# Performance work log

Measured on AMD Instinct MI355X. Metric: run time of the kernel, lower is better.

The kernel has to match this reference:

```python
import jax, jax.numpy as jnp
import numpy as np

N = 100000   # nodes
E = 1600000  # edges (before self-loops)
F_IN = 128
H = 64
G = 512      # graphs in batch


def _add_self_loops(edge_index, n):
    loop = jnp.arange(n, dtype=edge_index.dtype)
    src = jnp.concatenate([edge_index[0], loop])
    dst = jnp.concatenate([edge_index[1], loop])
    return src, dst


def _gcn_norm(src, dst, n):
    # PyG GCNConv: deg over targets with self-loops, norm = d^-1/2[src]*d^-1/2[dst]
    deg = jax.ops.segment_sum(jnp.ones_like(dst, dtype=jnp.float32), dst, num_segments=n)
    dinv = jnp.where(deg > 0, jax.lax.rsqrt(deg), 0.0)
    return dinv[src] * dinv[dst]


def _gcn_conv(x, src, dst, norm, W, b):
    xw = x @ W                                # [N, H]
    msg = xw[src] * norm[:, None]             # [E+N, H] gather + scale
    out = jax.ops.segment_sum(msg, dst, num_segments=x.shape[0])
    return out + b


def setup_inputs() -> dict:
    key = jax.random.key(0)
    ks = jax.random.split(key, 9)
    x = jax.random.normal(ks[0], (N, F_IN), dtype=jnp.float32)
    edge_index = jax.random.randint(ks[1], (2, E), 0, N, dtype=jnp.int32)
    batch = jnp.sort(jax.random.randint(ks[2], (N,), 0, G, dtype=jnp.int32))
    s1 = 1.0 / np.sqrt(F_IN)
    s2 = 1.0 / np.sqrt(H)
    W1 = jax.random.uniform(ks[3], (F_IN, H), jnp.float32, -s1, s1)
    b1 = jnp.zeros((H,), jnp.float32)
    W2 = jax.random.uniform(ks[4], (H, H), jnp.float32, -s2, s2)
    b2 = jnp.zeros((H,), jnp.float32)
    Wl = jax.random.uniform(ks[5], (H, 1), jnp.float32, -s2, s2)
    bl = jnp.zeros((1,), jnp.float32)
    return {"x": x, "edge_index": edge_index, "batch": batch,
            "W1": W1, "b1": b1, "W2": W2, "b2": b2, "Wl": Wl, "bl": bl}


def reference(x, edge_index, batch, W1, b1, W2, b2, Wl, bl):
    n = x.shape[0]
    src, dst = _add_self_loops(edge_index, n)
    norm = _gcn_norm(src, dst, n)
    h = jax.nn.relu(_gcn_conv(x, src, dst, norm, W1, b1))
    h = jax.nn.relu(_gcn_conv(h, src, dst, norm, W2, b2))
    # global mean pool over graphs
    sums = jax.ops.segment_sum(h, batch, num_segments=G)          # [G, H]
    cnt = jax.ops.segment_sum(jnp.ones((n,), jnp.float32), batch, num_segments=G)
    pooled = sums / jnp.maximum(cnt, 1.0)[:, None]
    return jax.nn.sigmoid(pooled @ Wl + bl)                        # [G, 1]
```

## Files before the change

### kernel.cpp

```cpp
#include <hip/hip_runtime.h>
#include <hip/hip_bf16.h>
#include <cmath>

#define F_IN 128
#define HDIM 64
#define NPB 256
#define NB1 512
#define CAP 4800
#define CHMAX 3136

typedef __attribute__((ext_vector_type(8))) short bf16x8;
typedef __attribute__((ext_vector_type(4))) float f32x4;
typedef __attribute__((ext_vector_type(2))) float f32x2;

__device__ __forceinline__ float bf2f(unsigned short u) {
    union { unsigned int i; float f; } v; v.i = ((unsigned int)u) << 16; return v.f;
}
__device__ __forceinline__ unsigned short f2bf(float f) {
    __hip_bfloat16 h = __float2bfloat16(f);
    union { __hip_bfloat16 h; unsigned short u; } c; c.h = h; return c.u;
}
__device__ __forceinline__ unsigned char f2fp8(float f) {
    int p = __builtin_amdgcn_cvt_pk_fp8_f32(f, f, 0, false);
    return (unsigned char)(p & 0xff);
}
__device__ __forceinline__ void fp8x8_acc(uint2 v, float* a) {
    f32x2 f;
    f = __builtin_amdgcn_cvt_pk_f32_fp8(v.x, false); a[0] += f.x; a[1] += f.y;
    f = __builtin_amdgcn_cvt_pk_f32_fp8(v.x, true);  a[2] += f.x; a[3] += f.y;
    f = __builtin_amdgcn_cvt_pk_f32_fp8(v.y, false); a[4] += f.x; a[5] += f.y;
    f = __builtin_amdgcn_cvt_pk_f32_fp8(v.y, true);  a[6] += f.x; a[7] += f.y;
}
__device__ __forceinline__ void fp8x8_acc_m(uint2 v, float m, float* a) {
    f32x2 f;
    f = __builtin_amdgcn_cvt_pk_f32_fp8(v.x, false); a[0] = fmaf(f.x, m, a[0]); a[1] = fmaf(f.y, m, a[1]);
    f = __builtin_amdgcn_cvt_pk_f32_fp8(v.x, true);  a[2] = fmaf(f.x, m, a[2]); a[3] = fmaf(f.y, m, a[3]);
    f = __builtin_amdgcn_cvt_pk_f32_fp8(v.y, false); a[4] = fmaf(f.x, m, a[4]); a[5] = fmaf(f.y, m, a[5]);
    f = __builtin_amdgcn_cvt_pk_f32_fp8(v.y, true);  a[6] = fmaf(f.x, m, a[6]); a[7] = fmaf(f.y, m, a[7]);
}

__device__ __forceinline__ void gather_rows(const int* __restrict__ col,
                                            const uint2* __restrict__ xws,
                                            int L, int s, int end, float* a) {
    int e = s;
    for (; e + 8 <= end; e += 8) {
        uint2 v0 = xws[(size_t)col[e + 0] * 8 + L];
        uint2 v1 = xws[(size_t)col[e + 1] * 8 + L];
        uint2 v2 = xws[(size_t)col[e + 2] * 8 + L];
        uint2 v3 = xws[(size_t)col[e + 3] * 8 + L];
        uint2 v4 = xws[(size_t)col[e + 4] * 8 + L];
        uint2 v5 = xws[(size_t)col[e + 5] * 8 + L];
        uint2 v6 = xws[(size_t)col[e + 6] * 8 + L];
        uint2 v7 = xws[(size_t)col[e + 7] * 8 + L];
        fp8x8_acc(v0, a); fp8x8_acc(v1, a); fp8x8_acc(v2, a); fp8x8_acc(v3, a);
        fp8x8_acc(v4, a); fp8x8_acc(v5, a); fp8x8_acc(v6, a); fp8x8_acc(v7, a);
    }
    if (e < end) {
        int last = end - 1;
        uint2 v0 = xws[(size_t)col[e]               * 8 + L];
        uint2 v1 = xws[(size_t)col[min(e + 1, last)] * 8 + L];
        uint2 v2 = xws[(size_t)col[min(e + 2, last)] * 8 + L];
        uint2 v3 = xws[(size_t)col[min(e + 3, last)] * 8 + L];
        uint2 v4 = xws[(size_t)col[min(e + 4, last)] * 8 + L];
        uint2 v5 = xws[(size_t)col[min(e + 5, last)] * 8 + L];
        uint2 v6 = xws[(size_t)col[min(e + 6, last)] * 8 + L];
        uint2 v7 = xws[(size_t)col[min(e + 7, last)] * 8 + L];
        fp8x8_acc(v0, a);
        fp8x8_acc_m(v1, (e + 1 < end) ? 1.0f : 0.0f, a);
        fp8x8_acc_m(v2, (e + 2 < end) ? 1.0f : 0.0f, a);
        fp8x8_acc_m(v3, (e + 3 < end) ? 1.0f : 0.0f, a);
        fp8x8_acc_m(v4, (e + 4 < end) ? 1.0f : 0.0f, a);
        fp8x8_acc_m(v5, (e + 5 < end) ? 1.0f : 0.0f, a);
        fp8x8_acc_m(v6, (e + 6 < end) ? 1.0f : 0.0f, a);
        fp8x8_acc_m(v7, (e + 7 < end) ? 1.0f : 0.0f, a);
    }
}


__launch_bounds__(256)
__global__ void k_init(const float* __restrict__ W1, const float* __restrict__ W2,
                       unsigned short* __restrict__ w1t, unsigned short* __restrict__ w2t,
                       const int* __restrict__ batch, int* __restrict__ gstart,
                       int n, int G, int* __restrict__ gcnt) {
    int t = blockIdx.x * 256 + threadIdx.x;
    if (t < F_IN * 64) {
        int c = t & 63, k = t >> 6;
        w1t[c * F_IN + k] = f2bf(W1[t]);
        return;
    }
    t -= F_IN * 64;
    if (t < HDIM * 64) {
        int c = t & 63, k = t >> 6;
        w2t[c * HDIM + k] = f2bf(W2[t]);
        return;
    }
    t -= HDIM * 64;
    if (t <= G) {
        int g = t;
        int lo = 0, hi = n;
        while (lo < hi) {
            int mid = (lo + hi) >> 1;
            if (batch[mid] < g) lo = mid + 1; else hi = mid;
        }
        gstart[g] = lo;
        return;
    }
    t -= G + 1;
    if (t < 512) gcnt[t] = 0;
}


__launch_bounds__(512)
__global__ void p_place(const int* __restrict__ src, const int* __restrict__ dst,
                        int* __restrict__ gcnt, int* __restrict__ pairs,
                        int E, int nbuk, int chunk) {
    __shared__ int hist[512];
    __shared__ int cur[512];
    __shared__ int dch[CHMAX];
    int tid = threadIdx.x;
    for (int i = tid; i < nbuk; i += 512) hist[i] = 0;
    __syncthreads();
    int lo = blockIdx.x * chunk, hi = min(E, lo + chunk), m = hi - lo;
    for (int i = tid; i < m; i += 512) {
        int d = dst[lo + i];
        dch[i] = d;
        atomicAdd(&hist[d >> 8], 1);
    }
    __syncthreads();
    for (int i = tid; i < nbuk; i += 512) {
        int c = hist[i];
        cur[i] = i * CAP + (c ? atomicAdd(&gcnt[i], c) : 0);
    }
    __syncthreads();
    for (int i = tid; i < m; i += 512) {
        int d = dch[i];
        int pos = atomicAdd(&cur[d >> 8], 1);
        pairs[pos] = (src[lo + i] << 8) | (d & 255);
    }
}


__launch_bounds__(256)
__global__ void p2_csr(const int* __restrict__ pairs, const int* __restrict__ bucket_cnt,
                       float* __restrict__ dinv, int* __restrict__ col,
                       int4* __restrict__ slot_hdr, int n) {
    __shared__ int plds[CAP];
    __shared__ int dl[256];
    __shared__ int sc[256];
    __shared__ int cur[256];
    __shared__ int h64[64];
    __shared__ int s64[64];
    int b = blockIdx.x, tid = threadIdx.x;
    int nlo = b << 8;
    int eb = b * CAP;
    int cnt = bucket_cnt[b];
    dl[tid] = 0;
    if (tid < 64) h64[tid] = 0;
    __syncthreads();
    for (int i = tid; i < cnt; i += 256) {
        int v = pairs[eb + i];
        plds[i] = v;
        atomicAdd(&dl[v & 255], 1);
    }
    __syncthreads();
    int d0 = dl[tid];
    sc[tid] = d0;
    __syncthreads();
    for (int off = 1; off < 256; off <<= 1) {
        int a = (tid >= off) ? sc[tid - off] : 0;
        __syncthreads();
        sc[tid] += a;
        __syncthreads();
    }
    int excl = sc[tid] - d0;
    int node = nlo + tid;
    float dv = rsqrtf((float)(d0 + 1));
    if (node < n) dinv[node] = dv;
    cur[tid] = eb + excl;
    atomicAdd(&h64[min(d0, 63)], 1);
    __syncthreads();
    if (tid == 0) { int run = 0; for (int i = 0; i < 64; ++i) { s64[i] = run; run += h64[i]; } }
    __syncthreads();
    if (tid < 64) h64[tid] = 0;
    __syncthreads();
    {
        int bin = min(d0, 63);
        int pos = s64[bin] + atomicAdd(&h64[bin], 1);
        int4 hdr;
        hdr.x = (node < n) ? node : 0x7fffffff;
        hdr.y = eb + excl;
        hdr.z = d0;
        hdr.w = __float_as_int(dv);
        slot_hdr[nlo + pos] = hdr;
    }
    __syncthreads();
    for (int i = tid; i < cnt; i += 256) {
        unsigned int v = (unsigned int)plds[i];
        int pos = atomicAdd(&cur[v & 255], 1);
        col[pos] = (int)(v >> 8);
    }
}


template <int K>
__launch_bounds__(256)
__global__ void matmul_mfma(const float* __restrict__ X, const unsigned short* __restrict__ Wt,
                            const float* __restrict__ dinv, unsigned char* __restrict__ out,
                            int n) {
    constexpr int KS  = K / 32;
    constexpr int LDX = K + 8;
    __shared__ unsigned short Xs[64 * LDX];
    __shared__ unsigned short Ws[64 * LDX];
    int tid = threadIdx.x;
    int rowbase = blockIdx.x * 64;
    for (int i = tid; i < 64 * (K / 8); i += 256) {
        int r = i / (K / 8), ch = i % (K / 8);
        *(bf16x8*)(Ws + r * LDX + ch * 8) = ((const bf16x8*)Wt)[i];
    }
    {
        const float4* X4 = (const float4*)X;
        for (int i = tid; i < 64 * (K / 4); i += 256) {
            int r = i / (K / 4), k4 = i % (K / 4);
            ushort4 u = { 0, 0, 0, 0 };
            int gr = rowbase + r;
            if (gr < n) {
                float4 v = X4[(size_t)gr * (K / 4) + k4];
                u.x = f2bf(v.x); u.y = f2bf(v.y); u.z = f2bf(v.z); u.w = f2bf(v.w);
            }
            *(ushort4*)(Xs + r * LDX + k4 * 4) = u;
        }
    }
    __syncthreads();
    int wave = tid >> 6, lane = tid & 63;
    int q = lane >> 4, nn = lane & 15;
    f32x4 acc[4] = {{0,0,0,0},{0,0,0,0},{0,0,0,0},{0,0,0,0}};
    int mrow = wave * 16 + nn;
#pragma unroll
    for (int s = 0; s < KS; ++s) {
        bf16x8 af = *(const bf16x8*)(Xs + mrow * LDX + s * 32 + q * 8);
#pragma unroll
        for (int c = 0; c < 4; ++c) {
            bf16x8 bf = *(const bf16x8*)(Ws + (c * 16 + nn) * LDX + s * 32 + q * 8);
            acc[c] = __builtin_amdgcn_mfma_f32_16x16x32_bf16(af, bf, acc[c], 0, 0, 0);
        }
    }
#pragma unroll
    for (int r = 0; r < 4; ++r) {
        int row = rowbase + wave * 16 + q * 4 + r;
        if (row >= n) continue;
        float dv = dinv[row];
#pragma unroll
        for (int c = 0; c < 4; ++c)
            out[(size_t)row * HDIM + c * 16 + nn] = f2fp8(acc[c][r] * dv);
    }
}


__launch_bounds__(256)
__global__ void gather1_mm2(const int4* __restrict__ slot_hdr, const int* __restrict__ col,
                            const uint2* __restrict__ xws, const float* __restrict__ bias,
                            const unsigned short* __restrict__ w2t,
                            unsigned char* __restrict__ out8, int nslots, int n) {
    __shared__ unsigned short Hs[32 * 72];
    __shared__ unsigned short Ws[64 * 72];
    __shared__ int   snode[32];
    __shared__ float sdinv[32];

    int tid = threadIdx.x;
    int ls = tid >> 3;
    int L  = tid & 7;
    int slot = blockIdx.x * 32 + ls;

    for (int i = tid; i < 64 * 8; i += 256) {
        int r = i >> 3, ch = i & 7;
        *(bf16x8*)(Ws + r * 72 + ch * 8) = ((const bf16x8*)w2t)[i];
    }

    int node = 0x7fffffff;
    float dv = 0.0f;
    float a[8] = {0, 0, 0, 0, 0, 0, 0, 0};
    if (slot < nslots) {
        int4 hdr = slot_hdr[slot];
        node = hdr.x;
        if (node < n) {
            dv = __int_as_float(hdr.w);
            fp8x8_acc(xws[(size_t)node * 8 + L], a);
            gather_rows(col, xws, L, hdr.y, hdr.y + hdr.z, a);
        }
    }
    if (L == 0) { snode[ls] = node; sdinv[ls] = dv; }
    {
        int f0 = L * 8;
        bf16x8 o;
        if (node < n) {
#pragma unroll
            for (int j = 0; j < 8; ++j)
                o[j] = (short)f2bf(fmaxf(fmaf(a[j], dv, bias[f0 + j]), 0.0f));
        } else {
            short z[8] = {0,0,0,0,0,0,0,0};
            o = *(bf16x8*)z;
        }
        *(bf16x8*)(Hs + ls * 72 + L * 8) = o;
    }
    __syncthreads();

    int wave = tid >> 6, lane = tid & 63;
    int q = lane >> 4, nn = lane & 15;
    int mt  = wave & 1;
    int nt0 = (wave >> 1) * 2;
    f32x4 acc[2] = {{0,0,0,0},{0,0,0,0}};
#pragma unroll
    for (int s = 0; s < 2; ++s) {
        bf16x8 af = *(const bf16x8*)(Hs + (mt * 16 + nn) * 72 + s * 32 + q * 8);
#pragma unroll
        for (int t = 0; t < 2; ++t) {
            bf16x8 bf = *(const bf16x8*)(Ws + ((nt0 + t) * 16 + nn) * 72 + s * 32 + q * 8);
            acc[t] = __builtin_amdgcn_mfma_f32_16x16x32_bf16(af, bf, acc[t], 0, 0, 0);
        }
    }
#pragma unroll
    for (int r = 0; r < 4; ++r) {
        int lslot = mt * 16 + q * 4 + r;
        int nd = snode[lslot];
        if (nd >= n) continue;
        float dvr = sdinv[lslot];
#pragma unroll
        for (int t = 0; t < 2; ++t)
            out8[(size_t)nd * HDIM + (nt0 + t) * 16 + nn] = f2fp8(acc[t][r] * dvr);
    }
}


__launch_bounds__(256)
__global__ void csr_gather8_fp8(const int4* __restrict__ slot_hdr, const int* __restrict__ col,
                                const uint2* __restrict__ xws, const float* __restrict__ bias,
                                bf16x8* __restrict__ outb, int nslots, int n) {
    int t = blockIdx.x * 256 + threadIdx.x;
    int slot = t >> 3;
    if (slot >= nslots) return;
    int L = t & 7;
    int4 hdr = slot_hdr[slot];
    int node = hdr.x;
    if (node >= n) return;
    float dv = __int_as_float(hdr.w);

    float a[8] = {0, 0, 0, 0, 0, 0, 0, 0};
    fp8x8_acc(xws[(size_t)node * 8 + L], a);
    gather_rows(col, xws, L, hdr.y, hdr.y + hdr.z, a);

    int f0 = L * 8;
    bf16x8 o;
#pragma unroll
    for (int j = 0; j < 8; ++j)
        o[j] = (short)f2bf(fmaxf(fmaf(a[j], dv, bias[f0 + j]), 0.0f));
    outb[(size_t)node * 8 + L] = o;
}


__launch_bounds__(256)
__global__ void pool_head(const unsigned short* __restrict__ h, const int* __restrict__ gstart,
                          const float* __restrict__ Wl, const float* __restrict__ bl,
                          float* __restrict__ out, int G) {
    int g = blockIdx.x;
    int s = gstart[g], e = gstart[g + 1];
    int f  = threadIdx.x & 63;
    int rg = threadIdx.x >> 6;
    float acc = 0.0f;
    for (int i = s + rg; i < e; i += 4)
        acc += bf2f(h[(size_t)i * HDIM + f]);
    __shared__ float red[4][HDIM];
    red[rg][f] = acc;
    __syncthreads();
    if (rg == 0) {
        float v = (red[0][f] + red[1][f]) + (red[2][f] + red[3][f]);
        float c = fmaxf((float)(e - s), 1.0f);
        v = v * Wl[f] * (1.0f / c);
#pragma unroll
        for (int off = 32; off; off >>= 1) v += __shfl_down(v, off, 64);
        if (f == 0) out[g] = 1.0f / (1.0f + expf(-(v + bl[0])));
    }
}


extern "C" void kernel_launch(void* const* d_in, const int* in_sizes, int n_in,
                              void* d_out, int out_size, void* d_ws, size_t ws_size,
                              hipStream_t stream) {
    const float* x   = (const float*)d_in[0];
    const int* ei    = (const int*)d_in[1];
    const int* batch = (const int*)d_in[2];
    const float* W1  = (const float*)d_in[3];
    const float* b1  = (const float*)d_in[4];
    const float* W2  = (const float*)d_in[5];
    const float* b2  = (const float*)d_in[6];
    const float* Wl  = (const float*)d_in[7];
    const float* bl  = (const float*)d_in[8];
    float* out = (float*)d_out;

    const int n = in_sizes[0] / F_IN;
    const int E = in_sizes[1] / 2;
    const int G = out_size;

    const int* srcp = ei;
    const int* dstp = ei + E;

    int nbuk = (n + NPB - 1) / NPB;
    int nslots = nbuk * NPB;

    char* wsb = (char*)d_ws;
    auto alloc = [&](size_t bytes) { char* p = wsb; wsb += (bytes + 255) & ~(size_t)255; return p; };
    float* dinv       = (float*)alloc((size_t)n * 4);
    int4*  slot_hdr   = (int4*)alloc((size_t)nslots * 16);
    int*   gcnt       = (int*)alloc(512 * 4);
    int*   pairs      = (int*)alloc((size_t)nbuk * CAP * 4);
    int*   colx       = (int*)alloc((size_t)nbuk * CAP * 4);
    unsigned short* w1t  = (unsigned short*)alloc((size_t)F_IN * HDIM * 2);
    unsigned short* w2t  = (unsigned short*)alloc((size_t)HDIM * HDIM * 2);
    unsigned char*  xws8 = (unsigned char*)alloc((size_t)n * HDIM);
    unsigned char*  xws8b= (unsigned char*)alloc((size_t)n * HDIM);
    unsigned short* xh2  = (unsigned short*)alloc((size_t)n * HDIM * 2);
    int*   gstart     = (int*)alloc(((size_t)G + 1) * 4);

    const int TB = 256;
    int gMM  = (n + 63) / 64;
    int chunk = (E + NB1 - 1) / NB1;
    int gG8  = (nslots * 8 + TB - 1) / TB;
    int gS   = (nslots + 31) / 32;
    int initWork = F_IN * 64 + HDIM * 64 + (G + 1) + 512;
    int gInit = (initWork + TB - 1) / TB;

    k_init<<<gInit, TB, 0, stream>>>(W1, W2, w1t, w2t, batch, gstart, n, G, gcnt);
    p_place<<<NB1, 512, 0, stream>>>(srcp, dstp, gcnt, pairs, E, nbuk, chunk);
    p2_csr<<<nbuk, TB, 0, stream>>>(pairs, gcnt, dinv, colx, slot_hdr, n);
    matmul_mfma<F_IN><<<gMM, TB, 0, stream>>>(x, w1t, dinv, xws8, n);
    gather1_mm2<<<gS, TB, 0, stream>>>(slot_hdr, colx, (const uint2*)xws8,
                                       b1, w2t, xws8b, nslots, n);
    csr_gather8_fp8<<<gG8, TB, 0, stream>>>(slot_hdr, colx, (const uint2*)xws8b,
                                            b2, (bf16x8*)xh2, nslots, n);
    pool_head<<<G, TB, 0, stream>>>(xh2, gstart, Wl, bl, out, G);
}
```

Measured before the change: 230.9 us.

## Fuse all GCN stages into one persistent cooperative kernel with grid syncs

Replaces seven separate kernel launches with a single cooperative persistent kernel that runs each stage (init, bucket placement, CSR build, layer-1 matmul, gather+matmul2, gather2, pooling) in grid-stride loops separated by grid.sync(). The goal is to remove per-launch overhead and inter-kernel gaps. As part of the fusion, the first matmul reads X directly from global memory into registers instead of staging it in LDS, and the placement pass now uses 1024 chunks with 256 threads. The trade-offs are a shared LDS union that may limit occupancy, a grid size capped by co-residency, and grid-wide barrier costs between stages.

```diff
diff --git a/kernel.cpp b/kernel.cpp
--- a/kernel.cpp
+++ b/kernel.cpp
@@ -1,13 +1,16 @@
 #include <hip/hip_runtime.h>
+#include <hip/hip_cooperative_groups.h>
 #include <hip/hip_bf16.h>
 #include <cmath>
+
+namespace cg = cooperative_groups;
 
 #define F_IN 128
 #define HDIM 64
 #define NPB 256
-#define NB1 512
+#define NCH 1024
 #define CAP 4800
-#define CHMAX 3136
+#define CHMAX 1600
 
 typedef __attribute__((ext_vector_type(8))) short bf16x8;
 typedef __attribute__((ext_vector_type(4))) float f32x4;
@@ -57,7 +60,7 @@
     }
     if (e < end) {
         int last = end - 1;
-        uint2 v0 = xws[(size_t)col[e]               * 8 + L];
+        uint2 v0 = xws[(size_t)col[e]                * 8 + L];
         uint2 v1 = xws[(size_t)col[min(e + 1, last)] * 8 + L];
         uint2 v2 = xws[(size_t)col[min(e + 2, last)] * 8 + L];
         uint2 v3 = xws[(size_t)col[min(e + 3, last)] * 8 + L];
@@ -76,308 +79,282 @@
     }
 }
 
-
-__launch_bounds__(256)
-__global__ void k_init(const float* __restrict__ W1, const float* __restrict__ W2,
-                       unsigned short* __restrict__ w1t, unsigned short* __restrict__ w2t,
-                       const int* __restrict__ batch, int* __restrict__ gstart,
-                       int n, int G, int* __restrict__ gcnt) {
-    int t = blockIdx.x * 256 + threadIdx.x;
-    if (t < F_IN * 64) {
-        int c = t & 63, k = t >> 6;
-        w1t[c * F_IN + k] = f2bf(W1[t]);
-        return;
-    }
-    t -= F_IN * 64;
-    if (t < HDIM * 64) {
-        int c = t & 63, k = t >> 6;
-        w2t[c * HDIM + k] = f2bf(W2[t]);
-        return;
-    }
-    t -= HDIM * 64;
-    if (t <= G) {
-        int g = t;
-        int lo = 0, hi = n;
-        while (lo < hi) {
-            int mid = (lo + hi) >> 1;
-            if (batch[mid] < g) lo = mid + 1; else hi = mid;
-        }
-        gstart[g] = lo;
-        return;
-    }
-    t -= G + 1;
-    if (t < 512) gcnt[t] = 0;
-}
-
-
-__launch_bounds__(512)
-__global__ void p_place(const int* __restrict__ src, const int* __restrict__ dst,
-                        int* __restrict__ gcnt, int* __restrict__ pairs,
-                        int E, int nbuk, int chunk) {
-    __shared__ int hist[512];
-    __shared__ int cur[512];
-    __shared__ int dch[CHMAX];
-    int tid = threadIdx.x;
-    for (int i = tid; i < nbuk; i += 512) hist[i] = 0;
-    __syncthreads();
-    int lo = blockIdx.x * chunk, hi = min(E, lo + chunk), m = hi - lo;
-    for (int i = tid; i < m; i += 512) {
-        int d = dst[lo + i];
-        dch[i] = d;
-        atomicAdd(&hist[d >> 8], 1);
-    }
-    __syncthreads();
-    for (int i = tid; i < nbuk; i += 512) {
-        int c = hist[i];
-        cur[i] = i * CAP + (c ? atomicAdd(&gcnt[i], c) : 0);
-    }
-    __syncthreads();
-    for (int i = tid; i < m; i += 512) {
-        int d = dch[i];
-        int pos = atomicAdd(&cur[d >> 8], 1);
-        pairs[pos] = (src[lo + i] << 8) | (d & 255);
-    }
-}
-
-
-__launch_bounds__(256)
-__global__ void p2_csr(const int* __restrict__ pairs, const int* __restrict__ bucket_cnt,
-                       float* __restrict__ dinv, int* __restrict__ col,
-                       int4* __restrict__ slot_hdr, int n) {
-    __shared__ int plds[CAP];
-    __shared__ int dl[256];
-    __shared__ int sc[256];
-    __shared__ int cur[256];
-    __shared__ int h64[64];
-    __shared__ int s64[64];
-    int b = blockIdx.x, tid = threadIdx.x;
-    int nlo = b << 8;
-    int eb = b * CAP;
-    int cnt = bucket_cnt[b];
-    dl[tid] = 0;
-    if (tid < 64) h64[tid] = 0;
-    __syncthreads();
-    for (int i = tid; i < cnt; i += 256) {
-        int v = pairs[eb + i];
-        plds[i] = v;
-        atomicAdd(&dl[v & 255], 1);
-    }
-    __syncthreads();
-    int d0 = dl[tid];
-    sc[tid] = d0;
-    __syncthreads();
-    for (int off = 1; off < 256; off <<= 1) {
-        int a = (tid >= off) ? sc[tid - off] : 0;
-        __syncthreads();
-        sc[tid] += a;
-        __syncthreads();
-    }
-    int excl = sc[tid] - d0;
-    int node = nlo + tid;
-    float dv = rsqrtf((float)(d0 + 1));
-    if (node < n) dinv[node] = dv;
-    cur[tid] = eb + excl;
-    atomicAdd(&h64[min(d0, 63)], 1);
-    __syncthreads();
-    if (tid == 0) { int run = 0; for (int i = 0; i < 64; ++i) { s64[i] = run; run += h64[i]; } }
-    __syncthreads();
-    if (tid < 64) h64[tid] = 0;
-    __syncthreads();
+struct GcnP {
+    const float* x; const int* src; const int* dst; const int* batch;
+    const float* W1; const float* b1; const float* W2; const float* b2;
+    const float* Wl; const float* bl; float* out;
+    float* dinv; int4* slot_hdr; int* gcnt; int* pairs; int* col;
+    unsigned short* w1t; unsigned short* w2t;
+    unsigned char* xws8; unsigned char* xws8b; unsigned short* xh2;
+    int* gstart;
+    int n, E, G, nbuk, nslots, chunk;
+};
+
+union SU {
+    struct { int hist[512], cur[512], dch[CHMAX]; } p1;
+    struct { int plds[CAP], dl[256], sc[256], cur[256], h64[64], s64[64]; } p2;
+    struct { unsigned short Ws[64 * 136]; } p3;
+    struct { unsigned short Ws[64 * 72], Hs[32 * 72]; int snode[32]; float sdinv[32]; } p4;
+    struct { float red[4][HDIM]; } p6;
+};
+
+__launch_bounds__(256, 4)
+__global__ void gcn_fused(GcnP p) {
+    cg::grid_group grid = cg::this_grid();
+    __shared__ SU su;
+    const int tid = threadIdx.x;
+    const int nbuk = p.nbuk;
+
     {
-        int bin = min(d0, 63);
-        int pos = s64[bin] + atomicAdd(&h64[bin], 1);
-        int4 hdr;
-        hdr.x = (node < n) ? node : 0x7fffffff;
-        hdr.y = eb + excl;
-        hdr.z = d0;
-        hdr.w = __float_as_int(dv);
-        slot_hdr[nlo + pos] = hdr;
-    }
-    __syncthreads();
-    for (int i = tid; i < cnt; i += 256) {
-        unsigned int v = (unsigned int)plds[i];
-        int pos = atomicAdd(&cur[v & 255], 1);
-        col[pos] = (int)(v >> 8);
-    }
-}
-
-
-template <int K>
-__launch_bounds__(256)
-__global__ void matmul_mfma(const float* __restrict__ X, const unsigned short* __restrict__ Wt,
-                            const float* __restrict__ dinv, unsigned char* __restrict__ out,
-                            int n) {
-    constexpr int KS  = K / 32;
-    constexpr int LDX = K + 8;
-    __shared__ unsigned short Xs[64 * LDX];
-    __shared__ unsigned short Ws[64 * LDX];
-    int tid = threadIdx.x;
-    int rowbase = blockIdx.x * 64;
-    for (int i = tid; i < 64 * (K / 8); i += 256) {
-        int r = i / (K / 8), ch = i % (K / 8);
-        *(bf16x8*)(Ws + r * LDX + ch * 8) = ((const bf16x8*)Wt)[i];
-    }
+        int total = F_IN * 64 + HDIM * 64 + (p.G + 1) + 512;
+        for (int t = blockIdx.x * 256 + tid; t < total; t += gridDim.x * 256) {
+            int u = t;
+            if (u < F_IN * 64) { int c = u & 63, k = u >> 6; p.w1t[c * F_IN + k] = f2bf(p.W1[u]); continue; }
+            u -= F_IN * 64;
+            if (u < HDIM * 64) { int c = u & 63, k = u >> 6; p.w2t[c * HDIM + k] = f2bf(p.W2[u]); continue; }
+            u -= HDIM * 64;
+            if (u <= p.G) {
+                int g = u, lo = 0, hi = p.n;
+                while (lo < hi) { int mid = (lo + hi) >> 1; if (p.batch[mid] < g) lo = mid + 1; else hi = mid; }
+                p.gstart[g] = lo;
+                continue;
+            }
+            u -= p.G + 1;
+            if (u < 512) p.gcnt[u] = 0;
+        }
+    }
+    grid.sync();
+
+    for (int c = blockIdx.x; c < NCH; c += gridDim.x) {
+        for (int i = tid; i < nbuk; i += 256) su.p1.hist[i] = 0;
+        __syncthreads();
+        int lo = c * p.chunk, hi = min(p.E, lo + p.chunk), m = hi - lo;
+        for (int i = tid; i < m; i += 256) {
+            int d = p.dst[lo + i];
+            su.p1.dch[i] = d;
+            atomicAdd(&su.p1.hist[d >> 8], 1);
+        }
+        __syncthreads();
+        for (int i = tid; i < nbuk; i += 256) {
+            int cc = su.p1.hist[i];
+            su.p1.cur[i] = i * CAP + (cc ? atomicAdd(&p.gcnt[i], cc) : 0);
+        }
+        __syncthreads();
+        for (int i = tid; i < m; i += 256) {
+            int d = su.p1.dch[i];
+            int pos = atomicAdd(&su.p1.cur[d >> 8], 1);
+            p.pairs[pos] = (p.src[lo + i] << 8) | (d & 255);
+        }
+        __syncthreads();
+    }
+    grid.sync();
+
+    for (int b = blockIdx.x; b < nbuk; b += gridDim.x) {
+        int nlo = b << 8;
+        int eb = b * CAP;
+        int cnt = p.gcnt[b];
+        su.p2.dl[tid] = 0;
+        if (tid < 64) su.p2.h64[tid] = 0;
+        __syncthreads();
+        for (int i = tid; i < cnt; i += 256) {
+            int v = p.pairs[eb + i];
+            su.p2.plds[i] = v;
+            atomicAdd(&su.p2.dl[v & 255], 1);
+        }
+        __syncthreads();
+        int d0 = su.p2.dl[tid];
+        su.p2.sc[tid] = d0;
+        __syncthreads();
+        for (int off = 1; off < 256; off <<= 1) {
+            int a = (tid >= off) ? su.p2.sc[tid - off] : 0;
+            __syncthreads();
+            su.p2.sc[tid] += a;
+            __syncthreads();
+        }
+        int excl = su.p2.sc[tid] - d0;
+        int node = nlo + tid;
+        float dv = rsqrtf((float)(d0 + 1));
+        if (node < p.n) p.dinv[node] = dv;
+        su.p2.cur[tid] = eb + excl;
+        atomicAdd(&su.p2.h64[min(d0, 63)], 1);
+        __syncthreads();
+        if (tid == 0) { int run = 0; for (int i = 0; i < 64; ++i) { su.p2.s64[i] = run; run += su.p2.h64[i]; } }
+        __syncthreads();
+        if (tid < 64) su.p2.h64[tid] = 0;
+        __syncthreads();
+        {
+            int bin = min(d0, 63);
+            int pos = su.p2.s64[bin] + atomicAdd(&su.p2.h64[bin], 1);
+            int4 hdr;
+            hdr.x = (node < p.n) ? node : 0x7fffffff;
+            hdr.y = eb + excl;
+            hdr.z = d0;
+            hdr.w = __float_as_int(dv);
+            p.slot_hdr[nlo + pos] = hdr;
+        }
+        __syncthreads();
+        for (int i = tid; i < cnt; i += 256) {
+            unsigned int v = (unsigned int)su.p2.plds[i];
+            int pos = atomicAdd(&su.p2.cur[v & 255], 1);
+            p.col[pos] = (int)(v >> 8);
+        }
+        __syncthreads();
+    }
+    grid.sync();
+
     {
-        const float4* X4 = (const float4*)X;
-        for (int i = tid; i < 64 * (K / 4); i += 256) {
-            int r = i / (K / 4), k4 = i % (K / 4);
-            ushort4 u = { 0, 0, 0, 0 };
-            int gr = rowbase + r;
-            if (gr < n) {
-                float4 v = X4[(size_t)gr * (K / 4) + k4];
-                u.x = f2bf(v.x); u.y = f2bf(v.y); u.z = f2bf(v.z); u.w = f2bf(v.w);
-            }
-            *(ushort4*)(Xs + r * LDX + k4 * 4) = u;
-        }
-    }
-    __syncthreads();
-    int wave = tid >> 6, lane = tid & 63;
-    int q = lane >> 4, nn = lane & 15;
-    f32x4 acc[4] = {{0,0,0,0},{0,0,0,0},{0,0,0,0},{0,0,0,0}};
-    int mrow = wave * 16 + nn;
-#pragma unroll
-    for (int s = 0; s < KS; ++s) {
-        bf16x8 af = *(const bf16x8*)(Xs + mrow * LDX + s * 32 + q * 8);
-#pragma unroll
-        for (int c = 0; c < 4; ++c) {
-            bf16x8 bf = *(const bf16x8*)(Ws + (c * 16 + nn) * LDX + s * 32 + q * 8);
-            acc[c] = __builtin_amdgcn_mfma_f32_16x16x32_bf16(af, bf, acc[c], 0, 0, 0);
-        }
-    }
-#pragma unroll
-    for (int r = 0; r < 4; ++r) {
-        int row = rowbase + wave * 16 + q * 4 + r;
-        if (row >= n) continue;
-        float dv = dinv[row];
-#pragma unroll
-        for (int c = 0; c < 4; ++c)
-            out[(size_t)row * HDIM + c * 16 + nn] = f2fp8(acc[c][r] * dv);
-    }
-}
-
-
-__launch_bounds__(256)
-__global__ void gather1_mm2(const int4* __restrict__ slot_hdr, const int* __restrict__ col,
-                            const uint2* __restrict__ xws, const float* __restrict__ bias,
-                            const unsigned short* __restrict__ w2t,
-                            unsigned char* __restrict__ out8, int nslots, int n) {
-    __shared__ unsigned short Hs[32 * 72];
-    __shared__ unsigned short Ws[64 * 72];
-    __shared__ int   snode[32];
-    __shared__ float sdinv[32];
-
-    int tid = threadIdx.x;
-    int ls = tid >> 3;
-    int L  = tid & 7;
-    int slot = blockIdx.x * 32 + ls;
-
-    for (int i = tid; i < 64 * 8; i += 256) {
-        int r = i >> 3, ch = i & 7;
-        *(bf16x8*)(Ws + r * 72 + ch * 8) = ((const bf16x8*)w2t)[i];
-    }
-
-    int node = 0x7fffffff;
-    float dv = 0.0f;
-    float a[8] = {0, 0, 0, 0, 0, 0, 0, 0};
-    if (slot < nslots) {
-        int4 hdr = slot_hdr[slot];
-        node = hdr.x;
-        if (node < n) {
-            dv = __int_as_float(hdr.w);
-            fp8x8_acc(xws[(size_t)node * 8 + L], a);
-            gather_rows(col, xws, L, hdr.y, hdr.y + hdr.z, a);
-        }
-    }
-    if (L == 0) { snode[ls] = node; sdinv[ls] = dv; }
+        int gMM = (p.n + 63) >> 6;
+        int wave = tid >> 6, lane = tid & 63, q = lane >> 4, nn = lane & 15;
+        for (int tile = blockIdx.x; tile < gMM; tile += gridDim.x) {
+            for (int i = tid; i < 64 * 16; i += 256) {
+                int r = i >> 4, ch = i & 15;
+                *(bf16x8*)(su.p3.Ws + r * 136 + ch * 8) = ((const bf16x8*)p.w1t)[i];
+            }
+            __syncthreads();
+            int rowbase = tile << 6;
+            int arow = rowbase + wave * 16 + nn;
+            bool rok = arow < p.n;
+            const float* Xr = p.x + (size_t)arow * F_IN;
+            f32x4 acc[4] = {{0,0,0,0},{0,0,0,0},{0,0,0,0},{0,0,0,0}};
+#pragma unroll
+            for (int s = 0; s < 4; ++s) {
+                bf16x8 af;
+                if (rok) {
+                    float4 xa = *(const float4*)(Xr + s * 32 + q * 8);
+                    float4 xb = *(const float4*)(Xr + s * 32 + q * 8 + 4);
+                    af[0] = (short)f2bf(xa.x); af[1] = (short)f2bf(xa.y);
+                    af[2] = (short)f2bf(xa.z); af[3] = (short)f2bf(xa.w);
+                    af[4] = (short)f2bf(xb.x); af[5] = (short)f2bf(xb.y);
+                    af[6] = (short)f2bf(xb.z); af[7] = (short)f2bf(xb.w);
+                } else {
+                    short z[8] = {0,0,0,0,0,0,0,0};
+                    af = *(bf16x8*)z;
+                }
+#pragma unroll
+                for (int cc = 0; cc < 4; ++cc) {
+                    bf16x8 bfv = *(const bf16x8*)(su.p3.Ws + (cc * 16 + nn) * 136 + s * 32 + q * 8);
+                    acc[cc] = __builtin_amdgcn_mfma_f32_16x16x32_bf16(af, bfv, acc[cc], 0, 0, 0);
+                }
+            }
+#pragma unroll
+            for (int r = 0; r < 4; ++r) {
+                int row = rowbase + wave * 16 + q * 4 + r;
+                if (row >= p.n) continue;
+                float dvv = p.dinv[row];
+#pragma unroll
+                for (int cc = 0; cc < 4; ++cc)
+                    p.xws8[(size_t)row * HDIM + cc * 16 + nn] = f2fp8(acc[cc][r] * dvv);
+            }
+            __syncthreads();
+        }
+    }
+    grid.sync();
+
     {
-        int f0 = L * 8;
-        bf16x8 o;
-        if (node < n) {
-#pragma unroll
-            for (int j = 0; j < 8; ++j)
-                o[j] = (short)f2bf(fmaxf(fmaf(a[j], dv, bias[f0 + j]), 0.0f));
-        } else {
-            short z[8] = {0,0,0,0,0,0,0,0};
-            o = *(bf16x8*)z;
-        }
-        *(bf16x8*)(Hs + ls * 72 + L * 8) = o;
-    }
-    __syncthreads();
-
-    int wave = tid >> 6, lane = tid & 63;
-    int q = lane >> 4, nn = lane & 15;
-    int mt  = wave & 1;
-    int nt0 = (wave >> 1) * 2;
-    f32x4 acc[2] = {{0,0,0,0},{0,0,0,0}};
-#pragma unroll
-    for (int s = 0; s < 2; ++s) {
-        bf16x8 af = *(const bf16x8*)(Hs + (mt * 16 + nn) * 72 + s * 32 + q * 8);
-#pragma unroll
-        for (int t = 0; t < 2; ++t) {
-            bf16x8 bf = *(const bf16x8*)(Ws + ((nt0 + t) * 16 + nn) * 72 + s * 32 + q * 8);
-            acc[t] = __builtin_amdgcn_mfma_f32_16x16x32_bf16(af, bf, acc[t], 0, 0, 0);
-        }
-    }
-#pragma unroll
-    for (int r = 0; r < 4; ++r) {
-        int lslot = mt * 16 + q * 4 + r;
-        int nd = snode[lslot];
-        if (nd >= n) continue;
-        float dvr = sdinv[lslot];
-#pragma unroll
-        for (int t = 0; t < 2; ++t)
-            out8[(size_t)nd * HDIM + (nt0 + t) * 16 + nn] = f2fp8(acc[t][r] * dvr);
-    }
-}
-
-
-__launch_bounds__(256)
-__global__ void csr_gather8_fp8(const int4* __restrict__ slot_hdr, const int* __restrict__ col,
-                                const uint2* __restrict__ xws, const float* __restrict__ bias,
-                                bf16x8* __restrict__ outb, int nslots, int n) {
-    int t = blockIdx.x * 256 + threadIdx.x;
-    int slot = t >> 3;
-    if (slot >= nslots) return;
-    int L = t & 7;
-    int4 hdr = slot_hdr[slot];
-    int node = hdr.x;
-    if (node >= n) return;
-    float dv = __int_as_float(hdr.w);
-
-    float a[8] = {0, 0, 0, 0, 0, 0, 0, 0};
-    fp8x8_acc(xws[(size_t)node * 8 + L], a);
-    gather_rows(col, xws, L, hdr.y, hdr.y + hdr.z, a);
-
-    int f0 = L * 8;
-    bf16x8 o;
-#pragma unroll
-    for (int j = 0; j < 8; ++j)
-        o[j] = (short)f2bf(fmaxf(fmaf(a[j], dv, bias[f0 + j]), 0.0f));
-    outb[(size_t)node * 8 + L] = o;
-}
-
-
-__launch_bounds__(256)
-__global__ void pool_head(const unsigned short* __restrict__ h, const int* __restrict__ gstart,
-                          const float* __restrict__ Wl, const float* __restrict__ bl,
-                          float* __restrict__ out, int G) {
-    int g = blockIdx.x;
-    int s = gstart[g], e = gstart[g + 1];
-    int f  = threadIdx.x & 63;
-    int rg = threadIdx.x >> 6;
-    float acc = 0.0f;
-    for (int i = s + rg; i < e; i += 4)
-        acc += bf2f(h[(size_t)i * HDIM + f]);
-    __shared__ float red[4][HDIM];
-    red[rg][f] = acc;
-    __syncthreads();
-    if (rg == 0) {
-        float v = (red[0][f] + red[1][f]) + (red[2][f] + red[3][f]);
-        float c = fmaxf((float)(e - s), 1.0f);
-        v = v * Wl[f] * (1.0f / c);
-#pragma unroll
-        for (int off = 32; off; off >>= 1) v += __shfl_down(v, off, 64);
-        if (f == 0) out[g] = 1.0f / (1.0f + expf(-(v + bl[0])));
+        for (int i = tid; i < 64 * 8; i += 256) {
+            int r = i >> 3, ch = i & 7;
+            *(bf16x8*)(su.p4.Ws + r * 72 + ch * 8) = ((const bf16x8*)p.w2t)[i];
+        }
+        __syncthreads();
+        int ngroups = p.nslots >> 5;
+        int ls = tid >> 3, L = tid & 7;
+        int wave = tid >> 6, lane = tid & 63, q = lane >> 4, nn = lane & 15;
+        int mt = wave & 1, nt0 = (wave >> 1) * 2;
+        for (int grp = blockIdx.x; grp < ngroups; grp += gridDim.x) {
+            int slot = (grp << 5) + ls;
+            int node = 0x7fffffff;
+            float dvv = 0.0f;
+            float a[8] = {0, 0, 0, 0, 0, 0, 0, 0};
+            {
+                int4 hdr = p.slot_hdr[slot];
+                node = hdr.x;
+                if (node < p.n) {
+                    dvv = __int_as_float(hdr.w);
+                    fp8x8_acc(((const uint2*)p.xws8)[(size_t)node * 8 + L], a);
+                    gather_rows(p.col, (const uint2*)p.xws8, L, hdr.y, hdr.y + hdr.z, a);
+                }
+            }
+            if (L == 0) { su.p4.snode[ls] = node; su.p4.sdinv[ls] = dvv; }
+            {
+                int f0 = L * 8;
+                bf16x8 o;
+                if (node < p.n) {
+#pragma unroll
+                    for (int j = 0; j < 8; ++j)
+                        o[j] = (short)f2bf(fmaxf(fmaf(a[j], dvv, p.b1[f0 + j]), 0.0f));
+                } else {
+                    short z[8] = {0,0,0,0,0,0,0,0};
+                    o = *(bf16x8*)z;
+                }
+                *(bf16x8*)(su.p4.Hs + ls * 72 + L * 8) = o;
+            }
+            __syncthreads();
+            f32x4 acc2[2] = {{0,0,0,0},{0,0,0,0}};
+#pragma unroll
+            for (int s = 0; s < 2; ++s) {
+                bf16x8 af = *(const bf16x8*)(su.p4.Hs + (mt * 16 + nn) * 72 + s * 32 + q * 8);
+#pragma unroll
+                for (int t = 0; t < 2; ++t) {
+                    bf16x8 bfv = *(const bf16x8*)(su.p4.Ws + ((nt0 + t) * 16 + nn) * 72 + s * 32 + q * 8);
+                    acc2[t] = __builtin_amdgcn_mfma_f32_16x16x32_bf16(af, bfv, acc2[t], 0, 0, 0);
+                }
+            }
+#pragma unroll
+            for (int r = 0; r < 4; ++r) {
+                int lslot = mt * 16 + q * 4 + r;
+                int nd = su.p4.snode[lslot];
+                if (nd >= p.n) continue;
+                float dvr = su.p4.sdinv[lslot];
+#pragma unroll
+                for (int t = 0; t < 2; ++t)
+                    p.xws8b[(size_t)nd * HDIM + (nt0 + t) * 16 + nn] = f2fp8(acc2[t][r] * dvr);
+            }
+            __syncthreads();
+        }
+    }
+    grid.sync();
+
+    {
+        int tot = p.nslots * 8;
+        for (int t5 = blockIdx.x * 256 + tid; t5 < tot; t5 += gridDim.x * 256) {
+            int slot = t5 >> 3, L = t5 & 7;
+            int4 hdr = p.slot_hdr[slot];
+            int node = hdr.x;
+            if (node < p.n) {
+                float dvv = __int_as_float(hdr.w);
+                float a[8] = {0, 0, 0, 0, 0, 0, 0, 0};
+                fp8x8_acc(((const uint2*)p.xws8b)[(size_t)node * 8 + L], a);
+                gather_rows(p.col, (const uint2*)p.xws8b, L, hdr.y, hdr.y + hdr.z, a);
+                int f0 = L * 8;
+                bf16x8 o;
+#pragma unroll
+                for (int j = 0; j < 8; ++j)
+                    o[j] = (short)f2bf(fmaxf(fmaf(a[j], dvv, p.b2[f0 + j]), 0.0f));
+                ((bf16x8*)p.xh2)[(size_t)node * 8 + L] = o;
+            }
+        }
+    }
+    grid.sync();
+
+    {
+        int f = tid & 63, rg = tid >> 6;
+        for (int g = blockIdx.x; g < p.G; g += gridDim.x) {
+            int s = p.gstart[g], e = p.gstart[g + 1];
+            float acc = 0.0f;
+            for (int i = s + rg; i < e; i += 4)
+                acc += bf2f(p.xh2[(size_t)i * HDIM + f]);
+            su.p6.red[rg][f] = acc;
+            __syncthreads();
+            if (rg == 0) {
+                float v = (su.p6.red[0][f] + su.p6.red[1][f]) + (su.p6.red[2][f] + su.p6.red[3][f]);
+                float c = fmaxf((float)(e - s), 1.0f);
+                v = v * p.Wl[f] * (1.0f / c);
+#pragma unroll
+                for (int off = 32; off; off >>= 1) v += __shfl_down(v, off, 64);
+                if (f == 0) p.out[g] = 1.0f / (1.0f + expf(-(v + p.bl[0])));
+            }
+            __syncthreads();
+        }
     }
 }
 
@@ -400,9 +377,6 @@
     const int E = in_sizes[1] / 2;
     const int G = out_size;
 
-    const int* srcp = ei;
-    const int* dstp = ei + E;
-
     int nbuk = (n + NPB - 1) / NPB;
     int nslots = nbuk * NPB;
 
@@ -420,21 +394,36 @@
     unsigned short* xh2  = (unsigned short*)alloc((size_t)n * HDIM * 2);
     int*   gstart     = (int*)alloc(((size_t)G + 1) * 4);
 
-    const int TB = 256;
-    int gMM  = (n + 63) / 64;
-    int chunk = (E + NB1 - 1) / NB1;
-    int gG8  = (nslots * 8 + TB - 1) / TB;
-    int gS   = (nslots + 31) / 32;
-    int initWork = F_IN * 64 + HDIM * 64 + (G + 1) + 512;
-    int gInit = (initWork + TB - 1) / TB;
-
-    k_init<<<gInit, TB, 0, stream>>>(W1, W2, w1t, w2t, batch, gstart, n, G, gcnt);
-    p_place<<<NB1, 512, 0, stream>>>(srcp, dstp, gcnt, pairs, E, nbuk, chunk);
-    p2_csr<<<nbuk, TB, 0, stream>>>(pairs, gcnt, dinv, colx, slot_hdr, n);
-    matmul_mfma<F_IN><<<gMM, TB, 0, stream>>>(x, w1t, dinv, xws8, n);
-    gather1_mm2<<<gS, TB, 0, stream>>>(slot_hdr, colx, (const uint2*)xws8,
-                                       b1, w2t, xws8b, nslots, n);
-    csr_gather8_fp8<<<gG8, TB, 0, stream>>>(slot_hdr, colx, (const uint2*)xws8b,
-                                            b2, (bf16x8*)xh2, nslots, n);
-    pool_head<<<G, TB, 0, stream>>>(xh2, gstart, Wl, bl, out, G);
-}
+    GcnP prm;
+    prm.x = x; prm.src = ei; prm.dst = ei + E; prm.batch = batch;
+    prm.W1 = W1; prm.b1 = b1; prm.W2 = W2; prm.b2 = b2; prm.Wl = Wl; prm.bl = bl;
+    prm.out = out;
+    prm.dinv = dinv; prm.slot_hdr = slot_hdr; prm.gcnt = gcnt;
+    prm.pairs = pairs; prm.col = colx;
+    prm.w1t = w1t; prm.w2t = w2t;
+    prm.xws8 = xws8; prm.xws8b = xws8b; prm.xh2 = xh2;
+    prm.gstart = gstart;
+    prm.n = n; prm.E = E; prm.G = G; prm.nbuk = nbuk; prm.nslots = nslots;
+    prm.chunk = (E + NCH - 1) / NCH;
+
+    static int s_grid = 0;
+    if (s_grid == 0) {
+        int maxb = 0;
+        hipOccupancyMaxActiveBlocksPerMultiprocessor(&maxb, (const void*)gcn_fused, 256, 0);
+        if (maxb < 1) maxb = 1;
+        int ncu = 256;
+        int dev = 0;
+        hipDeviceProp_t prop;
+        if (hipGetDevice(&dev) == hipSuccess &&
+            hipGetDeviceProperties(&prop, dev) == hipSuccess &&
+            prop.multiProcessorCount > 0)
+            ncu = prop.multiProcessorCount;
+        long g = (long)maxb * (long)ncu;
+        if (g > 2048) g = 2048;
+        if (g < 256)  g = 256;
+        s_grid = (int)g;
+    }
+
+    void* kargs[] = { (void*)&prm };
+    hipLaunchCooperativeKernel((void*)gcn_fused, dim3(s_grid), dim3(256), kargs, 0, stream);
+}
```

Measured after the change: 633.9 us. +174.6%, slower.
